# Kernel optimization log

Measured on AMD Instinct MI355X. Metric: run time of the kernel, lower is better.

Reference implementation:

```python
import jax, jax.numpy as jnp
import numpy as np

N_NODES = 50000
N_EDGES = 640000
D = 128  # input = hidden = output channels (must match for this module's forward to type-check)


def gcn_conv(x, W, b, src, dst, n):
    """PyG GCNConv: out = D^{-1/2} (A + I) D^{-1/2} (x @ W) + b.
    src = edge_index[0] (source/message sender), dst = edge_index[1] (target/aggregation index).
    """
    h = x @ W  # [n, d_out]
    loop = jnp.arange(n)
    s = jnp.concatenate([src, loop])  # add self-loops
    d = jnp.concatenate([dst, loop])
    deg = jax.ops.segment_sum(jnp.ones(s.shape[0], dtype=h.dtype), d, num_segments=n)
    dis = jax.lax.rsqrt(deg)  # deg >= 1 thanks to self-loops
    norm = dis[s] * dis[d]  # [E + n]
    msg = h[s] * norm[:, None]  # gather + scale (largest intermediate)
    return jax.ops.segment_sum(msg, d, num_segments=n) + b


def setup_inputs() -> dict:
    key = jax.random.key(0)
    ks = jax.random.split(key, 9)
    x = jax.random.normal(ks[0], (N_NODES, D), dtype=jnp.float32)
    edge_index_normal = jax.random.randint(ks[1], (2, N_EDGES), 0, N_NODES, dtype=jnp.int64 if jax.config.jax_enable_x64 else jnp.int32)
    edge_index_role = jax.random.randint(ks[2], (2, N_EDGES), 0, N_NODES, dtype=jnp.int64 if jax.config.jax_enable_x64 else jnp.int32)
    s = 1.0 / np.sqrt(D)
    W_role = jax.random.uniform(ks[3], (D, D), jnp.float32, -s, s)
    b_role = jnp.zeros((D,), jnp.float32)
    W2 = jax.random.uniform(ks[4], (D, D), jnp.float32, -s, s)
    b2 = jnp.zeros((D,), jnp.float32)
    W1 = jax.random.uniform(ks[5], (D, D), jnp.float32, -s, s)
    b1 = jnp.zeros((D,), jnp.float32)
    return {"x": x, "W_role": W_role, "b_role": b_role, "W2": W2, "b2": b2,
            "W1": W1, "b1": b1,
            "edge_index_normal": edge_index_normal, "edge_index_role": edge_index_role}


def reference(x, W_role, b_role, W2, b2, W1, b1, edge_index_normal, edge_index_role):
    n = x.shape[0]
    # conv_role on the role graph, then conv2 and conv1 on the normal graph.
    h = jax.nn.relu(gcn_conv(x, W_role, b_role, edge_index_role[0], edge_index_role[1], n))
    # dropout(p=0.5) is identity in eval mode
    h = jax.nn.relu(gcn_conv(h, W2, b2, edge_index_normal[0], edge_index_normal[1], n))
    out = gcn_conv(h, W1, b1, edge_index_normal[0], edge_index_normal[1], n)
    return out
```

## Files before the change

### kernel.cpp

```cpp
#include <hip/hip_runtime.h>
#include <hip/hip_fp16.h>

#define D 128
#define CHUNK 8192
#define BSH 7
#define BNODES 128
#define MAXNB 512
#define CAP 6144
#define PADK 136

typedef _Float16 half8 __attribute__((ext_vector_type(8)));
typedef float float4v __attribute__((ext_vector_type(4)));

__global__ __launch_bounds__(256) void p1_hist(const int* __restrict__ dst_n,
                                               const int* __restrict__ dst_r,
                                               int En, int Er,
                                               int* __restrict__ base2,
                                               int NB, int NC, int L) {
    int g = blockIdx.x / NC, c = blockIdx.x % NC;
    const int* dst = g ? dst_r : dst_n;
    int E = g ? Er : En;
    __shared__ int hist[MAXNB];
    for (int i = threadIdx.x; i < NB; i += 256) hist[i] = 0;
    __syncthreads();
    int e0 = c * CHUNK, e1 = min(e0 + CHUNK, E);
    for (int e = e0 + threadIdx.x; e < e1; e += 256)
        atomicAdd(&hist[dst[e] >> BSH], 1);
    __syncthreads();
    for (int b = threadIdx.x; b < NB; b += 256)
        base2[g * L + b * NC + c] = hist[b];
}

__global__ __launch_bounds__(1024) void scan_pass1(const int* __restrict__ data,
                                                   int* __restrict__ bsum2, int L, int nb) {
    int g = blockIdx.x / nb, b = blockIdx.x % nb;
    int i = b * 1024 + threadIdx.x;
    int v = (i < L) ? data[g * L + i] : 0;
    #pragma unroll
    for (int off = 32; off; off >>= 1) v += __shfl_down(v, off, 64);
    __shared__ int wsum[16];
    int lane = threadIdx.x & 63, wid = threadIdx.x >> 6;
    if (lane == 0) wsum[wid] = v;
    __syncthreads();
    if (threadIdx.x == 0) {
        int s = 0;
        for (int w = 0; w < 16; ++w) s += wsum[w];
        bsum2[g * 64 + b] = s;
    }
}

__global__ __launch_bounds__(128) void scan_pass2(int* __restrict__ bsum2, int nb) {
    int wid = threadIdx.x >> 6, lane = threadIdx.x & 63;
    int v = (lane < nb) ? bsum2[wid * 64 + lane] : 0;
    int incl = v;
    #pragma unroll
    for (int off = 1; off < 64; off <<= 1) {
        int t = __shfl_up(incl, off, 64);
        if (lane >= off) incl += t;
    }
    if (lane < nb) bsum2[wid * 64 + lane] = incl - v;
}

__global__ __launch_bounds__(1024) void scan_pass3(int* __restrict__ data,
                                                   const int* __restrict__ bsum2,
                                                   int L, int nb) {
    int g = blockIdx.x / nb, b = blockIdx.x % nb;
    int i = b * 1024 + threadIdx.x;
    int v = (i < L) ? data[g * L + i] : 0;
    int lane = threadIdx.x & 63, wid = threadIdx.x >> 6;
    int incl = v;
    #pragma unroll
    for (int off = 1; off < 64; off <<= 1) {
        int t = __shfl_up(incl, off, 64);
        if (lane >= off) incl += t;
    }
    __shared__ int wsum[16];
    if (lane == 63) wsum[wid] = incl;
    __syncthreads();
    if (threadIdx.x == 0) {
        int s = 0;
        for (int w = 0; w < 16; ++w) { int t = wsum[w]; wsum[w] = s; s += t; }
    }
    __syncthreads();
    if (i < L) data[g * L + i] = incl - v + wsum[wid] + bsum2[g * 64 + b];
}

__global__ __launch_bounds__(256) void p2_scatter(const int* __restrict__ src_n,
                                                  const int* __restrict__ dst_n,
                                                  const int* __restrict__ src_r,
                                                  const int* __restrict__ dst_r,
                                                  int En, int Er,
                                                  const int* __restrict__ base2,
                                                  unsigned int* __restrict__ part_n,
                                                  unsigned int* __restrict__ part_r,
                                                  int NB, int NC, int L) {
    int g = blockIdx.x / NC, c = blockIdx.x % NC;
    const int* src = g ? src_r : src_n;
    const int* dst = g ? dst_r : dst_n;
    unsigned int* part = g ? part_r : part_n;
    int E = g ? Er : En;
    __shared__ int cur[MAXNB];
    for (int b = threadIdx.x; b < NB; b += 256)
        cur[b] = base2[g * L + b * NC + c];
    __syncthreads();
    int e0 = c * CHUNK, e1 = min(e0 + CHUNK, E);
    for (int e = e0 + threadIdx.x; e < e1; e += 256) {
        int d = dst[e];
        int pos = atomicAdd(&cur[d >> BSH], 1);
        part[pos] = ((unsigned)d << 16) | (unsigned)src[e];
    }
}

__global__ __launch_bounds__(256) void p3_csr(const unsigned int* __restrict__ part_n,
                                              const unsigned int* __restrict__ part_r,
                                              const int* __restrict__ base2,
                                              int* __restrict__ rs2,
                                              float* __restrict__ dis2,
                                              unsigned short* __restrict__ csr_n,
                                              unsigned short* __restrict__ csr_r,
                                              int n, int NB, int NC, int L, int En, int Er) {
    int g = blockIdx.x / NB, b = blockIdx.x % NB;
    const unsigned int* part = g ? part_r : part_n;
    unsigned short* csr = g ? csr_r : csr_n;
    int E = g ? Er : En;
    __shared__ int deg[BNODES];
    __shared__ int cur[BNODES];
    __shared__ unsigned short buf[CAP];
    __shared__ int w0tot;
    int t = threadIdx.x;
    if (t < BNODES) deg[t] = 0;
    __syncthreads();
    int bstart = base2[g * L + b * NC];
    int bend = (b + 1 < NB) ? base2[g * L + (b + 1) * NC] : E;
    int sz = bend - bstart;
    for (int e = bstart + t; e < bend; e += 256)
        atomicAdd(&deg[(part[e] >> 16) & (BNODES - 1)], 1);
    __syncthreads();
    int incl = 0, v = 0;
    if (t < BNODES) {
        int lane = t & 63;
        v = deg[t];
        incl = v;
        #pragma unroll
        for (int off = 1; off < 64; off <<= 1) {
            int tt = __shfl_up(incl, off, 64);
            if (lane >= off) incl += tt;
        }
        if (t == 63) w0tot = incl;
    }
    __syncthreads();
    if (t < BNODES) {
        int excl = incl - v + ((t >= 64) ? w0tot : 0);
        cur[t] = excl;
        int idx = b * BNODES + t;
        if (idx < n) {
            rs2[g * (n + 1) + idx] = bstart + excl;
            dis2[g * n + idx] = rsqrtf((float)(deg[t] + 1));
        }
    }
    if (b == NB - 1 && t == 255) rs2[g * (n + 1) + n] = E;
    __syncthreads();
    if (sz <= CAP) {
        for (int e = bstart + t; e < bend; e += 256) {
            unsigned int p = part[e];
            int pos = atomicAdd(&cur[(p >> 16) & (BNODES - 1)], 1);
            buf[pos] = (unsigned short)(p & 0xffffu);
        }
        __syncthreads();
        for (int i = t; i < sz; i += 256) csr[bstart + i] = buf[i];
    } else {
        for (int e = bstart + t; e < bend; e += 256) {
            unsigned int p = part[e];
            int pos = atomicAdd(&cur[(p >> 16) & (BNODES - 1)], 1);
            csr[bstart + pos] = (unsigned short)(p & 0xffffu);
        }
    }
}

__global__ __launch_bounds__(256) void wprep(const float* __restrict__ W2,
                                             const float* __restrict__ W1,
                                             _Float16* __restrict__ Wt2,
                                             _Float16* __restrict__ Wt1) {
    int i = blockIdx.x * 256 + threadIdx.x;
    int m = i >> 14;
    int idx = i & 16383;
    int nn = idx >> 7, k = idx & 127;
    const float* W = m ? W1 : W2;
    _Float16* Wt = m ? Wt1 : Wt2;
    Wt[nn * 128 + k] = (_Float16)W[k * 128 + nn];
}


__global__ __launch_bounds__(256) void gemm_scale(const float* __restrict__ X,
                                                  const float* __restrict__ W,
                                                  const float* __restrict__ dis,
                                                  __half* __restrict__ Y, int n) {
    __shared__ float sX[128 * D];
    int t = threadIdx.x;
    int rg = t >> 4;
    int cg = (t & 15) << 3;
    int rb = blockIdx.x * 128;
    int rows = min(128, n - rb);

    float4* sX4 = (float4*)sX;
    for (int i = t; i < rows * 32; i += 256)
        sX4[i] = ((const float4*)X)[(size_t)rb * 32 + i];
    __syncthreads();

    float acc[8][8] = {};
    #pragma unroll 2
    for (int k0 = 0; k0 < D; k0 += 4) {
        float4 xr[8];
        #pragma unroll
        for (int r = 0; r < 8; ++r)
            xr[r] = *(const float4*)&sX[(rg * 8 + r) * D + k0];
        #pragma unroll
        for (int j = 0; j < 4; ++j) {
            float4 wa = *(const float4*)(W + (size_t)(k0 + j) * D + cg);
            float4 wb = *(const float4*)(W + (size_t)(k0 + j) * D + cg + 4);
            #pragma unroll
            for (int r = 0; r < 8; ++r) {
                float xv = ((const float*)&xr[r])[j];
                acc[r][0] += xv * wa.x; acc[r][1] += xv * wa.y;
                acc[r][2] += xv * wa.z; acc[r][3] += xv * wa.w;
                acc[r][4] += xv * wb.x; acc[r][5] += xv * wb.y;
                acc[r][6] += xv * wb.z; acc[r][7] += xv * wb.w;
            }
        }
    }
    #pragma unroll
    for (int r = 0; r < 8; ++r) {
        int row = rb + rg * 8 + r;
        if (row < n) {
            float dv = dis[row];
            __half2 p0 = __floats2half2_rn(acc[r][0] * dv, acc[r][1] * dv);
            __half2 p1 = __floats2half2_rn(acc[r][2] * dv, acc[r][3] * dv);
            __half2 p2 = __floats2half2_rn(acc[r][4] * dv, acc[r][5] * dv);
            __half2 p3 = __floats2half2_rn(acc[r][6] * dv, acc[r][7] * dv);
            uint4 o;
            o.x = *(unsigned*)&p0; o.y = *(unsigned*)&p1;
            o.z = *(unsigned*)&p2; o.w = *(unsigned*)&p3;
            *(uint4*)(Y + (size_t)row * D + cg) = o;
        }
    }
}

__global__ __launch_bounds__(256) void gemm_mfma(const _Float16* __restrict__ Xh,
                                                 const _Float16* __restrict__ Wt,
                                                 const float* __restrict__ dis,
                                                 _Float16* __restrict__ Y, int n) {
    __shared__ _Float16 sA[128 * PADK];
    __shared__ _Float16 sB[128 * PADK];
    int t = threadIdx.x;
    int rb = blockIdx.x * 128;
    int rows = min(128, n - rb);

    for (int i = t; i < 128 * 16; i += 256) {
        int r = i >> 4, s = i & 15;
        *(uint4*)&sB[r * PADK + s * 8] = ((const uint4*)Wt)[i];
    }
    for (int i = t; i < rows * 16; i += 256) {
        int r = i >> 4, s = i & 15;
        *(uint4*)&sA[r * PADK + s * 8] = ((const uint4*)(Xh + (size_t)rb * D))[i];
    }
    if (rows < 128) {
        for (int i = rows * 16 + t; i < 128 * 16; i += 256) {
            int r = i >> 4, s = i & 15;
            *(uint4*)&sA[r * PADK + s * 8] = make_uint4(0, 0, 0, 0);
        }
    }
    __syncthreads();

    int w = t >> 6, lane = t & 63;
    int quad = lane >> 4, l16 = lane & 15;
    float4v acc[2][8];
    #pragma unroll
    for (int rt = 0; rt < 2; ++rt)
        #pragma unroll
        for (int ct = 0; ct < 8; ++ct)
            acc[rt][ct] = (float4v){0.f, 0.f, 0.f, 0.f};

    #pragma unroll
    for (int k0 = 0; k0 < 128; k0 += 32) {
        half8 a0 = *(half8*)&sA[(w * 32 + l16) * PADK + k0 + quad * 8];
        half8 a1 = *(half8*)&sA[(w * 32 + 16 + l16) * PADK + k0 + quad * 8];
        #pragma unroll
        for (int ct = 0; ct < 8; ++ct) {
            half8 b = *(half8*)&sB[(ct * 16 + l16) * PADK + k0 + quad * 8];
            acc[0][ct] = __builtin_amdgcn_mfma_f32_16x16x32_f16(a0, b, acc[0][ct], 0, 0, 0);
            acc[1][ct] = __builtin_amdgcn_mfma_f32_16x16x32_f16(a1, b, acc[1][ct], 0, 0, 0);
        }
    }
    #pragma unroll
    for (int rt = 0; rt < 2; ++rt) {
        #pragma unroll
        for (int r = 0; r < 4; ++r) {
            int row = rb + w * 32 + rt * 16 + quad * 4 + r;
            if (row < n) {
                float dv = dis[row];
                #pragma unroll
                for (int ct = 0; ct < 8; ++ct)
                    Y[(size_t)row * D + ct * 16 + l16] = (_Float16)(acc[rt][ct][r] * dv);
            }
        }
    }
}

__global__ __launch_bounds__(256) void aggregate(const __half* __restrict__ g,
                                                 const int* __restrict__ rs,
                                                 const unsigned short* __restrict__ csr,
                                                 const float* __restrict__ dis,
                                                 const float* __restrict__ bias,
                                                 float* __restrict__ outf,
                                                 _Float16* __restrict__ outh,
                                                 int n, int do_relu, int write_half) {
    int v = blockIdx.x * 16 + (threadIdx.x >> 4);
    if (v >= n) return;
    int l16 = threadIdx.x & 15;
    const uint4* g4 = (const uint4*)g;
    float acc[8];
    {
        uint4 raw = g4[(size_t)v * 16 + l16];
        float2 f0 = __half22float2(*(__half2*)&raw.x);
        float2 f1 = __half22float2(*(__half2*)&raw.y);
        float2 f2 = __half22float2(*(__half2*)&raw.z);
        float2 f3 = __half22float2(*(__half2*)&raw.w);
        acc[0] = f0.x; acc[1] = f0.y; acc[2] = f1.x; acc[3] = f1.y;
        acc[4] = f2.x; acc[5] = f2.y; acc[6] = f3.x; acc[7] = f3.y;
    }
    int e = rs[v], end = rs[v + 1];
    while (e < end) {
        int m = min(16, end - e);
        int sid = (e + l16 < end) ? (int)csr[e + l16] : 0;
        int j = 0;
        for (; j + 7 < m; j += 8) {
            uint4 raw[8];
            #pragma unroll
            for (int u = 0; u < 8; ++u) {
                int s = __shfl(sid, j + u, 16);
                raw[u] = g4[(size_t)s * 16 + l16];
            }
            #pragma unroll
            for (int u = 0; u < 8; ++u) {
                float2 f0 = __half22float2(*(__half2*)&raw[u].x);
                float2 f1 = __half22float2(*(__half2*)&raw[u].y);
                float2 f2 = __half22float2(*(__half2*)&raw[u].z);
                float2 f3 = __half22float2(*(__half2*)&raw[u].w);
                acc[0] += f0.x; acc[1] += f0.y; acc[2] += f1.x; acc[3] += f1.y;
                acc[4] += f2.x; acc[5] += f2.y; acc[6] += f3.x; acc[7] += f3.y;
            }
        }
        for (; j + 3 < m; j += 4) {
            uint4 raw[4];
            #pragma unroll
            for (int u = 0; u < 4; ++u) {
                int s = __shfl(sid, j + u, 16);
                raw[u] = g4[(size_t)s * 16 + l16];
            }
            #pragma unroll
            for (int u = 0; u < 4; ++u) {
                float2 f0 = __half22float2(*(__half2*)&raw[u].x);
                float2 f1 = __half22float2(*(__half2*)&raw[u].y);
                float2 f2 = __half22float2(*(__half2*)&raw[u].z);
                float2 f3 = __half22float2(*(__half2*)&raw[u].w);
                acc[0] += f0.x; acc[1] += f0.y; acc[2] += f1.x; acc[3] += f1.y;
                acc[4] += f2.x; acc[5] += f2.y; acc[6] += f3.x; acc[7] += f3.y;
            }
        }
        for (; j < m; ++j) {
            int s = __shfl(sid, j, 16);
            uint4 raw = g4[(size_t)s * 16 + l16];
            float2 f0 = __half22float2(*(__half2*)&raw.x);
            float2 f1 = __half22float2(*(__half2*)&raw.y);
            float2 f2 = __half22float2(*(__half2*)&raw.z);
            float2 f3 = __half22float2(*(__half2*)&raw.w);
            acc[0] += f0.x; acc[1] += f0.y; acc[2] += f1.x; acc[3] += f1.y;
            acc[4] += f2.x; acc[5] += f2.y; acc[6] += f3.x; acc[7] += f3.y;
        }
        e += m;
    }
    float dv = dis[v];
    const float4* b4 = (const float4*)bias;
    float4 ba = b4[2 * l16], bb = b4[2 * l16 + 1];
    float o[8];
    o[0] = dv * acc[0] + ba.x; o[1] = dv * acc[1] + ba.y;
    o[2] = dv * acc[2] + ba.z; o[3] = dv * acc[3] + ba.w;
    o[4] = dv * acc[4] + bb.x; o[5] = dv * acc[5] + bb.y;
    o[6] = dv * acc[6] + bb.z; o[7] = dv * acc[7] + bb.w;
    if (do_relu) {
        #pragma unroll
        for (int i = 0; i < 8; ++i) o[i] = fmaxf(o[i], 0.f);
    }
    if (write_half) {
        __half2 p0 = __floats2half2_rn(o[0], o[1]);
        __half2 p1 = __floats2half2_rn(o[2], o[3]);
        __half2 p2 = __floats2half2_rn(o[4], o[5]);
        __half2 p3 = __floats2half2_rn(o[6], o[7]);
        uint4 pk;
        pk.x = *(unsigned*)&p0; pk.y = *(unsigned*)&p1;
        pk.z = *(unsigned*)&p2; pk.w = *(unsigned*)&p3;
        ((uint4*)outh)[(size_t)v * 16 + l16] = pk;
    } else {
        float4* orow = (float4*)(outf + (size_t)v * D);
        orow[2 * l16] = make_float4(o[0], o[1], o[2], o[3]);
        orow[2 * l16 + 1] = make_float4(o[4], o[5], o[6], o[7]);
    }
}


extern "C" void kernel_launch(void* const* d_in, const int* in_sizes, int n_in,
                              void* d_out, int out_size, void* d_ws, size_t ws_size,
                              hipStream_t stream) {
    const float* x      = (const float*)d_in[0];
    const float* W_role = (const float*)d_in[1];
    const float* b_role = (const float*)d_in[2];
    const float* W2     = (const float*)d_in[3];
    const float* b2     = (const float*)d_in[4];
    const float* W1     = (const float*)d_in[5];
    const float* b1     = (const float*)d_in[6];
    const int*   ein    = (const int*)d_in[7];
    const int*   eir    = (const int*)d_in[8];

    int n  = in_sizes[0] / D;
    int En = in_sizes[7] / 2;
    int Er = in_sizes[8] / 2;
    const int* src_n = ein;
    const int* dst_n = ein + En;
    const int* src_r = eir;
    const int* dst_r = eir + Er;
    float* out = (float*)d_out;

    int NB = (n + BNODES - 1) >> BSH;
    int Emax = En > Er ? En : Er;
    int NC = (Emax + CHUNK - 1) / CHUNK;
    int L  = NB * NC;
    int nb_scan = (L + 1023) / 1024;

    char* p = (char*)d_ws;
    auto alloc = [&](size_t bytes) { char* r = p; p += (bytes + 255) & ~(size_t)255; return r; };
    __half*         gbuf   = (__half*)alloc((size_t)n * D * sizeof(__half));
    _Float16*       hbuf   = (_Float16*)alloc((size_t)n * D * sizeof(_Float16));
    _Float16*       Wt2    = (_Float16*)alloc((size_t)D * D * sizeof(_Float16));
    _Float16*       Wt1    = (_Float16*)alloc((size_t)D * D * sizeof(_Float16));
    float*          dis2   = (float*)alloc((size_t)2 * n * sizeof(float));
    int*            rs2    = (int*)alloc((size_t)2 * (n + 1) * sizeof(int));
    int*            base2  = (int*)alloc((size_t)2 * L * sizeof(int));
    int*            bsum2  = (int*)alloc(512);
    unsigned int*   part_n = (unsigned int*)alloc((size_t)En * sizeof(unsigned int));
    unsigned int*   part_r = (unsigned int*)alloc((size_t)Er * sizeof(unsigned int));
    unsigned short* csr    = (unsigned short*)alloc((size_t)(En + Er) * sizeof(unsigned short));
    float* dis_n = dis2;
    float* dis_r = dis2 + n;
    int*   rs_n  = rs2;
    int*   rs_r  = rs2 + (n + 1);
    unsigned short* csr_n = csr;
    unsigned short* csr_r = csr + En;

    p1_hist<<<2 * NC, 256, 0, stream>>>(dst_n, dst_r, En, Er, base2, NB, NC, L);
    scan_pass1<<<2 * nb_scan, 1024, 0, stream>>>(base2, bsum2, L, nb_scan);
    scan_pass2<<<1, 128, 0, stream>>>(bsum2, nb_scan);
    scan_pass3<<<2 * nb_scan, 1024, 0, stream>>>(base2, bsum2, L, nb_scan);
    p2_scatter<<<2 * NC, 256, 0, stream>>>(src_n, dst_n, src_r, dst_r, En, Er,
                                           base2, part_n, part_r, NB, NC, L);
    p3_csr<<<2 * NB, 256, 0, stream>>>(part_n, part_r, base2, rs2, dis2,
                                       csr_n, csr_r, n, NB, NC, L, En, Er);
    wprep<<<128, 256, 0, stream>>>(W2, W1, Wt2, Wt1);

    int gblk = (n + 127) / 128;
    int ablk = (n + 15) / 16;
    gemm_scale<<<gblk, 256, 0, stream>>>(x, W_role, dis_r, gbuf, n);
    aggregate<<<ablk, 256, 0, stream>>>(gbuf, rs_r, csr_r, dis_r, b_role,
                                        nullptr, hbuf, n, 1, 1);
    gemm_mfma<<<gblk, 256, 0, stream>>>(hbuf, Wt2, dis_n, (_Float16*)gbuf, n);
    aggregate<<<ablk, 256, 0, stream>>>(gbuf, rs_n, csr_n, dis_n, b2,
                                        nullptr, hbuf, n, 1, 1);
    gemm_mfma<<<gblk, 256, 0, stream>>>(hbuf, Wt1, dis_n, (_Float16*)gbuf, n);
    aggregate<<<ablk, 256, 0, stream>>>(gbuf, rs_n, csr_n, dis_n, b1,
                                        out, nullptr, n, 0, 0);
}
```

Measured before the change: 270.0 us.

## Fuse CSR preprocessing and weight prep into one cooperative kernel

Merges the histogram, three-pass scan, scatter, CSR build and weight transpose/convert kernels into one cooperatively launched kernel separated by grid-wide syncs. The scan is rewritten to 256 threads with 4 elements each. The aim is to remove the launch and inter-kernel drain overhead of seven small kernels. In exchange, the CSR build stage now runs in a grid-stride loop over only 2*NC blocks instead of one block per bucket, which lowers parallelism, and each grid.sync adds its own cost.

```diff
diff --git a/kernel.cpp b/kernel.cpp
--- a/kernel.cpp
+++ b/kernel.cpp
@@ -1,5 +1,8 @@
 #include <hip/hip_runtime.h>
 #include <hip/hip_fp16.h>
+#include <hip/hip_cooperative_groups.h>
+
+namespace cg = cooperative_groups;
 
 #define D 128
 #define CHUNK 8192
@@ -12,182 +15,199 @@
 typedef _Float16 half8 __attribute__((ext_vector_type(8)));
 typedef float float4v __attribute__((ext_vector_type(4)));
 
-__global__ __launch_bounds__(256) void p1_hist(const int* __restrict__ dst_n,
-                                               const int* __restrict__ dst_r,
-                                               int En, int Er,
-                                               int* __restrict__ base2,
-                                               int NB, int NC, int L) {
-    int g = blockIdx.x / NC, c = blockIdx.x % NC;
-    const int* dst = g ? dst_r : dst_n;
-    int E = g ? Er : En;
-    __shared__ int hist[MAXNB];
-    for (int i = threadIdx.x; i < NB; i += 256) hist[i] = 0;
-    __syncthreads();
-    int e0 = c * CHUNK, e1 = min(e0 + CHUNK, E);
-    for (int e = e0 + threadIdx.x; e < e1; e += 256)
-        atomicAdd(&hist[dst[e] >> BSH], 1);
-    __syncthreads();
-    for (int b = threadIdx.x; b < NB; b += 256)
-        base2[g * L + b * NC + c] = hist[b];
-}
-
-__global__ __launch_bounds__(1024) void scan_pass1(const int* __restrict__ data,
-                                                   int* __restrict__ bsum2, int L, int nb) {
-    int g = blockIdx.x / nb, b = blockIdx.x % nb;
-    int i = b * 1024 + threadIdx.x;
-    int v = (i < L) ? data[g * L + i] : 0;
-    #pragma unroll
-    for (int off = 32; off; off >>= 1) v += __shfl_down(v, off, 64);
-    __shared__ int wsum[16];
-    int lane = threadIdx.x & 63, wid = threadIdx.x >> 6;
-    if (lane == 0) wsum[wid] = v;
-    __syncthreads();
-    if (threadIdx.x == 0) {
+__global__ __launch_bounds__(256) void preproc(
+    const int* __restrict__ src_n, const int* __restrict__ dst_n,
+    const int* __restrict__ src_r, const int* __restrict__ dst_r,
+    int En, int Er,
+    const float* __restrict__ W2, const float* __restrict__ W1,
+    _Float16* __restrict__ Wt2, _Float16* __restrict__ Wt1,
+    int* __restrict__ base2, int* __restrict__ bsum2,
+    unsigned int* __restrict__ part_n, unsigned int* __restrict__ part_r,
+    int* __restrict__ rs2, float* __restrict__ dis2,
+    unsigned short* __restrict__ csr_n, unsigned short* __restrict__ csr_r,
+    int n, int NB, int NC, int L, int nb_scan)
+{
+    cg::grid_group grid = cg::this_grid();
+    __shared__ __align__(16) char smem[14336];
+    int t = threadIdx.x;
+    int nblk = gridDim.x;
+
+    for (int i = blockIdx.x * 256 + t; i < 2 * 128 * 128; i += nblk * 256) {
+        int m = i >> 14, idx = i & 16383;
+        int nn = idx >> 7, k = idx & 127;
+        const float* W = m ? W1 : W2;
+        _Float16* Wt = m ? Wt1 : Wt2;
+        Wt[nn * 128 + k] = (_Float16)W[k * 128 + nn];
+    }
+
+    {
+        int g = blockIdx.x / NC, c = blockIdx.x % NC;
+        int* hist = (int*)smem;
+        const int* dst = g ? dst_r : dst_n;
+        int E = g ? Er : En;
+        for (int i = t; i < NB; i += 256) hist[i] = 0;
+        __syncthreads();
+        int e0 = c * CHUNK, e1 = min(e0 + CHUNK, E);
+        for (int e = e0 + t; e < e1; e += 256)
+            atomicAdd(&hist[dst[e] >> BSH], 1);
+        __syncthreads();
+        for (int b = t; b < NB; b += 256)
+            base2[g * L + b * NC + c] = hist[b];
+    }
+    grid.sync();
+
+    for (int task = blockIdx.x; task < 2 * nb_scan; task += nblk) {
+        int g = task / nb_scan, b = task % nb_scan;
+        int base = b * 1024 + t * 4;
         int s = 0;
-        for (int w = 0; w < 16; ++w) s += wsum[w];
-        bsum2[g * 64 + b] = s;
-    }
-}
-
-__global__ __launch_bounds__(128) void scan_pass2(int* __restrict__ bsum2, int nb) {
-    int wid = threadIdx.x >> 6, lane = threadIdx.x & 63;
-    int v = (lane < nb) ? bsum2[wid * 64 + lane] : 0;
-    int incl = v;
-    #pragma unroll
-    for (int off = 1; off < 64; off <<= 1) {
-        int t = __shfl_up(incl, off, 64);
-        if (lane >= off) incl += t;
-    }
-    if (lane < nb) bsum2[wid * 64 + lane] = incl - v;
-}
-
-__global__ __launch_bounds__(1024) void scan_pass3(int* __restrict__ data,
-                                                   const int* __restrict__ bsum2,
-                                                   int L, int nb) {
-    int g = blockIdx.x / nb, b = blockIdx.x % nb;
-    int i = b * 1024 + threadIdx.x;
-    int v = (i < L) ? data[g * L + i] : 0;
-    int lane = threadIdx.x & 63, wid = threadIdx.x >> 6;
-    int incl = v;
-    #pragma unroll
-    for (int off = 1; off < 64; off <<= 1) {
-        int t = __shfl_up(incl, off, 64);
-        if (lane >= off) incl += t;
-    }
-    __shared__ int wsum[16];
-    if (lane == 63) wsum[wid] = incl;
-    __syncthreads();
-    if (threadIdx.x == 0) {
-        int s = 0;
-        for (int w = 0; w < 16; ++w) { int t = wsum[w]; wsum[w] = s; s += t; }
-    }
-    __syncthreads();
-    if (i < L) data[g * L + i] = incl - v + wsum[wid] + bsum2[g * 64 + b];
-}
-
-__global__ __launch_bounds__(256) void p2_scatter(const int* __restrict__ src_n,
-                                                  const int* __restrict__ dst_n,
-                                                  const int* __restrict__ src_r,
-                                                  const int* __restrict__ dst_r,
-                                                  int En, int Er,
-                                                  const int* __restrict__ base2,
-                                                  unsigned int* __restrict__ part_n,
-                                                  unsigned int* __restrict__ part_r,
-                                                  int NB, int NC, int L) {
-    int g = blockIdx.x / NC, c = blockIdx.x % NC;
-    const int* src = g ? src_r : src_n;
-    const int* dst = g ? dst_r : dst_n;
-    unsigned int* part = g ? part_r : part_n;
-    int E = g ? Er : En;
-    __shared__ int cur[MAXNB];
-    for (int b = threadIdx.x; b < NB; b += 256)
-        cur[b] = base2[g * L + b * NC + c];
-    __syncthreads();
-    int e0 = c * CHUNK, e1 = min(e0 + CHUNK, E);
-    for (int e = e0 + threadIdx.x; e < e1; e += 256) {
-        int d = dst[e];
-        int pos = atomicAdd(&cur[d >> BSH], 1);
-        part[pos] = ((unsigned)d << 16) | (unsigned)src[e];
-    }
-}
-
-__global__ __launch_bounds__(256) void p3_csr(const unsigned int* __restrict__ part_n,
-                                              const unsigned int* __restrict__ part_r,
-                                              const int* __restrict__ base2,
-                                              int* __restrict__ rs2,
-                                              float* __restrict__ dis2,
-                                              unsigned short* __restrict__ csr_n,
-                                              unsigned short* __restrict__ csr_r,
-                                              int n, int NB, int NC, int L, int En, int Er) {
-    int g = blockIdx.x / NB, b = blockIdx.x % NB;
-    const unsigned int* part = g ? part_r : part_n;
-    unsigned short* csr = g ? csr_r : csr_n;
-    int E = g ? Er : En;
-    __shared__ int deg[BNODES];
-    __shared__ int cur[BNODES];
-    __shared__ unsigned short buf[CAP];
-    __shared__ int w0tot;
-    int t = threadIdx.x;
-    if (t < BNODES) deg[t] = 0;
-    __syncthreads();
-    int bstart = base2[g * L + b * NC];
-    int bend = (b + 1 < NB) ? base2[g * L + (b + 1) * NC] : E;
-    int sz = bend - bstart;
-    for (int e = bstart + t; e < bend; e += 256)
-        atomicAdd(&deg[(part[e] >> 16) & (BNODES - 1)], 1);
-    __syncthreads();
-    int incl = 0, v = 0;
-    if (t < BNODES) {
-        int lane = t & 63;
-        v = deg[t];
-        incl = v;
+        #pragma unroll
+        for (int j = 0; j < 4; ++j) {
+            int i = base + j;
+            if (i < L) s += base2[g * L + i];
+        }
+        int lane = t & 63, wid = t >> 6;
+        #pragma unroll
+        for (int off = 32; off; off >>= 1) s += __shfl_down(s, off, 64);
+        int* wsum = (int*)smem;
+        if (lane == 0) wsum[wid] = s;
+        __syncthreads();
+        if (t == 0) {
+            int tot = 0;
+            for (int w = 0; w < 4; ++w) tot += wsum[w];
+            bsum2[g * 64 + b] = tot;
+        }
+        __syncthreads();
+    }
+    grid.sync();
+
+    if (blockIdx.x == 0 && t < 128) {
+        int wid = t >> 6, lane = t & 63;
+        int v = (lane < nb_scan) ? bsum2[wid * 64 + lane] : 0;
+        int incl = v;
         #pragma unroll
         for (int off = 1; off < 64; off <<= 1) {
             int tt = __shfl_up(incl, off, 64);
             if (lane >= off) incl += tt;
         }
-        if (t == 63) w0tot = incl;
-    }
-    __syncthreads();
-    if (t < BNODES) {
-        int excl = incl - v + ((t >= 64) ? w0tot : 0);
-        cur[t] = excl;
-        int idx = b * BNODES + t;
-        if (idx < n) {
-            rs2[g * (n + 1) + idx] = bstart + excl;
-            dis2[g * n + idx] = rsqrtf((float)(deg[t] + 1));
-        }
-    }
-    if (b == NB - 1 && t == 255) rs2[g * (n + 1) + n] = E;
-    __syncthreads();
-    if (sz <= CAP) {
-        for (int e = bstart + t; e < bend; e += 256) {
-            unsigned int p = part[e];
-            int pos = atomicAdd(&cur[(p >> 16) & (BNODES - 1)], 1);
-            buf[pos] = (unsigned short)(p & 0xffffu);
-        }
-        __syncthreads();
-        for (int i = t; i < sz; i += 256) csr[bstart + i] = buf[i];
-    } else {
-        for (int e = bstart + t; e < bend; e += 256) {
-            unsigned int p = part[e];
-            int pos = atomicAdd(&cur[(p >> 16) & (BNODES - 1)], 1);
-            csr[bstart + pos] = (unsigned short)(p & 0xffffu);
-        }
-    }
-}
-
-__global__ __launch_bounds__(256) void wprep(const float* __restrict__ W2,
-                                             const float* __restrict__ W1,
-                                             _Float16* __restrict__ Wt2,
-                                             _Float16* __restrict__ Wt1) {
-    int i = blockIdx.x * 256 + threadIdx.x;
-    int m = i >> 14;
-    int idx = i & 16383;
-    int nn = idx >> 7, k = idx & 127;
-    const float* W = m ? W1 : W2;
-    _Float16* Wt = m ? Wt1 : Wt2;
-    Wt[nn * 128 + k] = (_Float16)W[k * 128 + nn];
+        if (lane < nb_scan) bsum2[wid * 64 + lane] = incl - v;
+    }
+    grid.sync();
+
+    for (int task = blockIdx.x; task < 2 * nb_scan; task += nblk) {
+        int g = task / nb_scan, b = task % nb_scan;
+        int base = b * 1024 + t * 4;
+        int v[4];
+        #pragma unroll
+        for (int j = 0; j < 4; ++j) {
+            int i = base + j;
+            v[j] = (i < L) ? base2[g * L + i] : 0;
+        }
+        int tsum = v[0] + v[1] + v[2] + v[3];
+        int lane = t & 63, wid = t >> 6;
+        int incl = tsum;
+        #pragma unroll
+        for (int off = 1; off < 64; off <<= 1) {
+            int tt = __shfl_up(incl, off, 64);
+            if (lane >= off) incl += tt;
+        }
+        int* wsum = (int*)smem;
+        if (lane == 63) wsum[wid] = incl;
+        __syncthreads();
+        if (t == 0) {
+            int s = 0;
+            for (int w = 0; w < 4; ++w) { int tt = wsum[w]; wsum[w] = s; s += tt; }
+        }
+        __syncthreads();
+        int excl = incl - tsum + wsum[wid] + bsum2[g * 64 + b];
+        #pragma unroll
+        for (int j = 0; j < 4; ++j) {
+            int i = base + j;
+            if (i < L) base2[g * L + i] = excl;
+            excl += v[j];
+        }
+        __syncthreads();
+    }
+    grid.sync();
+
+    {
+        int g = blockIdx.x / NC, c = blockIdx.x % NC;
+        const int* src = g ? src_r : src_n;
+        const int* dst = g ? dst_r : dst_n;
+        unsigned int* part = g ? part_r : part_n;
+        int E = g ? Er : En;
+        int* cur = (int*)smem;
+        for (int b = t; b < NB; b += 256)
+            cur[b] = base2[g * L + b * NC + c];
+        __syncthreads();
+        int e0 = c * CHUNK, e1 = min(e0 + CHUNK, E);
+        for (int e = e0 + t; e < e1; e += 256) {
+            int d = dst[e];
+            int pos = atomicAdd(&cur[d >> BSH], 1);
+            part[pos] = ((unsigned)d << 16) | (unsigned)src[e];
+        }
+    }
+    grid.sync();
+
+    {
+        int* deg = (int*)smem;
+        int* cur = deg + 128;
+        int* w0tot = cur + 128;
+        unsigned short* buf = (unsigned short*)(w0tot + 4);
+        for (int task = blockIdx.x; task < 2 * NB; task += nblk) {
+            int g = task / NB, b = task % NB;
+            const unsigned int* part = g ? part_r : part_n;
+            unsigned short* csr = g ? csr_r : csr_n;
+            int E = g ? Er : En;
+            if (t < BNODES) deg[t] = 0;
+            __syncthreads();
+            int bstart = base2[g * L + b * NC];
+            int bend = (b + 1 < NB) ? base2[g * L + (b + 1) * NC] : E;
+            int sz = bend - bstart;
+            for (int e = bstart + t; e < bend; e += 256)
+                atomicAdd(&deg[(part[e] >> 16) & (BNODES - 1)], 1);
+            __syncthreads();
+            int incl = 0, v = 0;
+            if (t < BNODES) {
+                int lane = t & 63;
+                v = deg[t];
+                incl = v;
+                #pragma unroll
+                for (int off = 1; off < 64; off <<= 1) {
+                    int tt = __shfl_up(incl, off, 64);
+                    if (lane >= off) incl += tt;
+                }
+                if (t == 63) w0tot[0] = incl;
+            }
+            __syncthreads();
+            if (t < BNODES) {
+                int excl = incl - v + ((t >= 64) ? w0tot[0] : 0);
+                cur[t] = excl;
+                int idx = b * BNODES + t;
+                if (idx < n) {
+                    rs2[g * (n + 1) + idx] = bstart + excl;
+                    dis2[g * n + idx] = rsqrtf((float)(deg[t] + 1));
+                }
+            }
+            if (b == NB - 1 && t == 255) rs2[g * (n + 1) + n] = E;
+            __syncthreads();
+            if (sz <= CAP) {
+                for (int e = bstart + t; e < bend; e += 256) {
+                    unsigned int p = part[e];
+                    int pos = atomicAdd(&cur[(p >> 16) & (BNODES - 1)], 1);
+                    buf[pos] = (unsigned short)(p & 0xffffu);
+                }
+                __syncthreads();
+                for (int i = t; i < sz; i += 256) csr[bstart + i] = buf[i];
+            } else {
+                for (int e = bstart + t; e < bend; e += 256) {
+                    unsigned int p = part[e];
+                    int pos = atomicAdd(&cur[(p >> 16) & (BNODES - 1)], 1);
+                    csr[bstart + pos] = (unsigned short)(p & 0xffffu);
+                }
+            }
+            __syncthreads();
+        }
+    }
 }
 
 
@@ -456,15 +476,20 @@
     unsigned short* csr_n = csr;
     unsigned short* csr_r = csr + En;
 
-    p1_hist<<<2 * NC, 256, 0, stream>>>(dst_n, dst_r, En, Er, base2, NB, NC, L);
-    scan_pass1<<<2 * nb_scan, 1024, 0, stream>>>(base2, bsum2, L, nb_scan);
-    scan_pass2<<<1, 128, 0, stream>>>(bsum2, nb_scan);
-    scan_pass3<<<2 * nb_scan, 1024, 0, stream>>>(base2, bsum2, L, nb_scan);
-    p2_scatter<<<2 * NC, 256, 0, stream>>>(src_n, dst_n, src_r, dst_r, En, Er,
-                                           base2, part_n, part_r, NB, NC, L);
-    p3_csr<<<2 * NB, 256, 0, stream>>>(part_n, part_r, base2, rs2, dis2,
-                                       csr_n, csr_r, n, NB, NC, L, En, Er);
-    wprep<<<128, 256, 0, stream>>>(W2, W1, Wt2, Wt1);
+    {
+        void* args[] = {
+            (void*)&src_n, (void*)&dst_n, (void*)&src_r, (void*)&dst_r,
+            (void*)&En, (void*)&Er,
+            (void*)&W2, (void*)&W1, (void*)&Wt2, (void*)&Wt1,
+            (void*)&base2, (void*)&bsum2,
+            (void*)&part_n, (void*)&part_r,
+            (void*)&rs2, (void*)&dis2,
+            (void*)&csr_n, (void*)&csr_r,
+            (void*)&n, (void*)&NB, (void*)&NC, (void*)&L, (void*)&nb_scan
+        };
+        hipLaunchCooperativeKernel((const void*)preproc, dim3(2 * NC), dim3(256),
+                                   args, 0, stream);
+    }
 
     int gblk = (n + 127) / 128;
     int ablk = (n + 15) / 16;
```

After: 399.5 us. 48.0% more time.

## Use MFMA for first-layer GEMM and fuse small prep kernels

Applied to the files above, without the earlier changes.

Replaces the scalar FP32 first-layer GEMM with an MFMA fp16 kernel that converts x to half while staging it in shared memory. The weight transpose/convert for all three matrices moves into the histogram kernel, and the second scan pass is folded into the third, which removes two launches. CHUNK is halved so there are more histogram/scatter blocks. Converting x to fp16 before the first GEMM adds rounding error, and the CHUNK change alters how parallel the partitioning passes are.

```diff
diff --git a/kernel.cpp b/kernel.cpp
--- a/kernel.cpp
+++ b/kernel.cpp
@@ -2,7 +2,7 @@
 #include <hip/hip_fp16.h>
 
 #define D 128
-#define CHUNK 8192
+#define CHUNK 4096
 #define BSH 7
 #define BNODES 128
 #define MAXNB 512
@@ -15,8 +15,21 @@
 __global__ __launch_bounds__(256) void p1_hist(const int* __restrict__ dst_n,
                                                const int* __restrict__ dst_r,
                                                int En, int Er,
+                                               const float* __restrict__ Wr,
+                                               const float* __restrict__ W2,
+                                               const float* __restrict__ W1,
+                                               _Float16* __restrict__ Wtr,
+                                               _Float16* __restrict__ Wt2,
+                                               _Float16* __restrict__ Wt1,
                                                int* __restrict__ base2,
                                                int NB, int NC, int L) {
+    for (int i = blockIdx.x * 256 + threadIdx.x; i < 3 * 128 * 128; i += gridDim.x * 256) {
+        int m = i >> 14, idx = i & 16383;
+        int nn = idx >> 7, k = idx & 127;
+        const float* W = (m == 0) ? Wr : (m == 1) ? W2 : W1;
+        _Float16* Wt = (m == 0) ? Wtr : (m == 1) ? Wt2 : Wt1;
+        Wt[nn * 128 + k] = (_Float16)W[k * 128 + nn];
+    }
     int g = blockIdx.x / NC, c = blockIdx.x % NC;
     const int* dst = g ? dst_r : dst_n;
     int E = g ? Er : En;
@@ -49,22 +62,22 @@
     }
 }
 
-__global__ __launch_bounds__(128) void scan_pass2(int* __restrict__ bsum2, int nb) {
-    int wid = threadIdx.x >> 6, lane = threadIdx.x & 63;
-    int v = (lane < nb) ? bsum2[wid * 64 + lane] : 0;
-    int incl = v;
-    #pragma unroll
-    for (int off = 1; off < 64; off <<= 1) {
-        int t = __shfl_up(incl, off, 64);
-        if (lane >= off) incl += t;
-    }
-    if (lane < nb) bsum2[wid * 64 + lane] = incl - v;
-}
-
 __global__ __launch_bounds__(1024) void scan_pass3(int* __restrict__ data,
                                                    const int* __restrict__ bsum2,
                                                    int L, int nb) {
     int g = blockIdx.x / nb, b = blockIdx.x % nb;
+    __shared__ int sOffset;
+    if (threadIdx.x < 64) {
+        int lane = threadIdx.x;
+        int v = (lane < nb) ? bsum2[g * 64 + lane] : 0;
+        int incl = v;
+        #pragma unroll
+        for (int off = 1; off < 64; off <<= 1) {
+            int t = __shfl_up(incl, off, 64);
+            if (lane >= off) incl += t;
+        }
+        if (lane == b) sOffset = incl - v;
+    }
     int i = b * 1024 + threadIdx.x;
     int v = (i < L) ? data[g * L + i] : 0;
     int lane = threadIdx.x & 63, wid = threadIdx.x >> 6;
@@ -82,7 +95,7 @@
         for (int w = 0; w < 16; ++w) { int t = wsum[w]; wsum[w] = s; s += t; }
     }
     __syncthreads();
-    if (i < L) data[g * L + i] = incl - v + wsum[wid] + bsum2[g * 64 + b];
+    if (i < L) data[g * L + i] = incl - v + wsum[wid] + sOffset;
 }
 
 __global__ __launch_bounds__(256) void p2_scatter(const int* __restrict__ src_n,
@@ -177,73 +190,6 @@
     }
 }
 
-__global__ __launch_bounds__(256) void wprep(const float* __restrict__ W2,
-                                             const float* __restrict__ W1,
-                                             _Float16* __restrict__ Wt2,
-                                             _Float16* __restrict__ Wt1) {
-    int i = blockIdx.x * 256 + threadIdx.x;
-    int m = i >> 14;
-    int idx = i & 16383;
-    int nn = idx >> 7, k = idx & 127;
-    const float* W = m ? W1 : W2;
-    _Float16* Wt = m ? Wt1 : Wt2;
-    Wt[nn * 128 + k] = (_Float16)W[k * 128 + nn];
-}
-
-
-__global__ __launch_bounds__(256) void gemm_scale(const float* __restrict__ X,
-                                                  const float* __restrict__ W,
-                                                  const float* __restrict__ dis,
-                                                  __half* __restrict__ Y, int n) {
-    __shared__ float sX[128 * D];
-    int t = threadIdx.x;
-    int rg = t >> 4;
-    int cg = (t & 15) << 3;
-    int rb = blockIdx.x * 128;
-    int rows = min(128, n - rb);
-
-    float4* sX4 = (float4*)sX;
-    for (int i = t; i < rows * 32; i += 256)
-        sX4[i] = ((const float4*)X)[(size_t)rb * 32 + i];
-    __syncthreads();
-
-    float acc[8][8] = {};
-    #pragma unroll 2
-    for (int k0 = 0; k0 < D; k0 += 4) {
-        float4 xr[8];
-        #pragma unroll
-        for (int r = 0; r < 8; ++r)
-            xr[r] = *(const float4*)&sX[(rg * 8 + r) * D + k0];
-        #pragma unroll
-        for (int j = 0; j < 4; ++j) {
-            float4 wa = *(const float4*)(W + (size_t)(k0 + j) * D + cg);
-            float4 wb = *(const float4*)(W + (size_t)(k0 + j) * D + cg + 4);
-            #pragma unroll
-            for (int r = 0; r < 8; ++r) {
-                float xv = ((const float*)&xr[r])[j];
-                acc[r][0] += xv * wa.x; acc[r][1] += xv * wa.y;
-                acc[r][2] += xv * wa.z; acc[r][3] += xv * wa.w;
-                acc[r][4] += xv * wb.x; acc[r][5] += xv * wb.y;
-                acc[r][6] += xv * wb.z; acc[r][7] += xv * wb.w;
-            }
-        }
-    }
-    #pragma unroll
-    for (int r = 0; r < 8; ++r) {
-        int row = rb + rg * 8 + r;
-        if (row < n) {
-            float dv = dis[row];
-            __half2 p0 = __floats2half2_rn(acc[r][0] * dv, acc[r][1] * dv);
-            __half2 p1 = __floats2half2_rn(acc[r][2] * dv, acc[r][3] * dv);
-            __half2 p2 = __floats2half2_rn(acc[r][4] * dv, acc[r][5] * dv);
-            __half2 p3 = __floats2half2_rn(acc[r][6] * dv, acc[r][7] * dv);
-            uint4 o;
-            o.x = *(unsigned*)&p0; o.y = *(unsigned*)&p1;
-            o.z = *(unsigned*)&p2; o.w = *(unsigned*)&p3;
-            *(uint4*)(Y + (size_t)row * D + cg) = o;
-        }
-    }
-}
 
 __global__ __launch_bounds__(256) void gemm_mfma(const _Float16* __restrict__ Xh,
                                                  const _Float16* __restrict__ Wt,
@@ -262,6 +208,72 @@
     for (int i = t; i < rows * 16; i += 256) {
         int r = i >> 4, s = i & 15;
         *(uint4*)&sA[r * PADK + s * 8] = ((const uint4*)(Xh + (size_t)rb * D))[i];
+    }
+    if (rows < 128) {
+        for (int i = rows * 16 + t; i < 128 * 16; i += 256) {
+            int r = i >> 4, s = i & 15;
+            *(uint4*)&sA[r * PADK + s * 8] = make_uint4(0, 0, 0, 0);
+        }
+    }
+    __syncthreads();
+
+    int w = t >> 6, lane = t & 63;
+    int quad = lane >> 4, l16 = lane & 15;
+    float4v acc[2][8];
+    #pragma unroll
+    for (int rt = 0; rt < 2; ++rt)
+        #pragma unroll
+        for (int ct = 0; ct < 8; ++ct)
+            acc[rt][ct] = (float4v){0.f, 0.f, 0.f, 0.f};
+
+    #pragma unroll
+    for (int k0 = 0; k0 < 128; k0 += 32) {
+        half8 a0 = *(half8*)&sA[(w * 32 + l16) * PADK + k0 + quad * 8];
+        half8 a1 = *(half8*)&sA[(w * 32 + 16 + l16) * PADK + k0 + quad * 8];
+        #pragma unroll
+        for (int ct = 0; ct < 8; ++ct) {
+            half8 b = *(half8*)&sB[(ct * 16 + l16) * PADK + k0 + quad * 8];
+            acc[0][ct] = __builtin_amdgcn_mfma_f32_16x16x32_f16(a0, b, acc[0][ct], 0, 0, 0);
+            acc[1][ct] = __builtin_amdgcn_mfma_f32_16x16x32_f16(a1, b, acc[1][ct], 0, 0, 0);
+        }
+    }
+    #pragma unroll
+    for (int rt = 0; rt < 2; ++rt) {
+        #pragma unroll
+        for (int r = 0; r < 4; ++r) {
+            int row = rb + w * 32 + rt * 16 + quad * 4 + r;
+            if (row < n) {
+                float dv = dis[row];
+                #pragma unroll
+                for (int ct = 0; ct < 8; ++ct)
+                    Y[(size_t)row * D + ct * 16 + l16] = (_Float16)(acc[rt][ct][r] * dv);
+            }
+        }
+    }
+}
+
+__global__ __launch_bounds__(256) void gemm_mfma_x(const float* __restrict__ X,
+                                                   const _Float16* __restrict__ Wt,
+                                                   const float* __restrict__ dis,
+                                                   _Float16* __restrict__ Y, int n) {
+    __shared__ _Float16 sA[128 * PADK];
+    __shared__ _Float16 sB[128 * PADK];
+    int t = threadIdx.x;
+    int rb = blockIdx.x * 128;
+    int rows = min(128, n - rb);
+
+    for (int i = t; i < 128 * 16; i += 256) {
+        int r = i >> 4, s = i & 15;
+        *(uint4*)&sB[r * PADK + s * 8] = ((const uint4*)Wt)[i];
+    }
+    for (int i = t; i < rows * 16; i += 256) {
+        int r = i >> 4, s = i & 15;
+        const float* xp = X + (size_t)(rb + r) * D + s * 8;
+        float4 a = *(const float4*)xp;
+        float4 b = *(const float4*)(xp + 4);
+        _Float16 h[8] = {(_Float16)a.x, (_Float16)a.y, (_Float16)a.z, (_Float16)a.w,
+                         (_Float16)b.x, (_Float16)b.y, (_Float16)b.z, (_Float16)b.w};
+        *(half8*)&sA[r * PADK + s * 8] = *(half8*)h;
     }
     if (rows < 128) {
         for (int i = rows * 16 + t; i < 128 * 16; i += 256) {
@@ -440,6 +452,7 @@
     auto alloc = [&](size_t bytes) { char* r = p; p += (bytes + 255) & ~(size_t)255; return r; };
     __half*         gbuf   = (__half*)alloc((size_t)n * D * sizeof(__half));
     _Float16*       hbuf   = (_Float16*)alloc((size_t)n * D * sizeof(_Float16));
+    _Float16*       Wtr    = (_Float16*)alloc((size_t)D * D * sizeof(_Float16));
     _Float16*       Wt2    = (_Float16*)alloc((size_t)D * D * sizeof(_Float16));
     _Float16*       Wt1    = (_Float16*)alloc((size_t)D * D * sizeof(_Float16));
     float*          dis2   = (float*)alloc((size_t)2 * n * sizeof(float));
@@ -456,19 +469,19 @@
     unsigned short* csr_n = csr;
     unsigned short* csr_r = csr + En;
 
-    p1_hist<<<2 * NC, 256, 0, stream>>>(dst_n, dst_r, En, Er, base2, NB, NC, L);
+    p1_hist<<<2 * NC, 256, 0, stream>>>(dst_n, dst_r, En, Er,
+                                        W_role, W2, W1, Wtr, Wt2, Wt1,
+                                        base2, NB, NC, L);
     scan_pass1<<<2 * nb_scan, 1024, 0, stream>>>(base2, bsum2, L, nb_scan);
-    scan_pass2<<<1, 128, 0, stream>>>(bsum2, nb_scan);
     scan_pass3<<<2 * nb_scan, 1024, 0, stream>>>(base2, bsum2, L, nb_scan);
     p2_scatter<<<2 * NC, 256, 0, stream>>>(src_n, dst_n, src_r, dst_r, En, Er,
                                            base2, part_n, part_r, NB, NC, L);
     p3_csr<<<2 * NB, 256, 0, stream>>>(part_n, part_r, base2, rs2, dis2,
                                        csr_n, csr_r, n, NB, NC, L, En, Er);
-    wprep<<<128, 256, 0, stream>>>(W2, W1, Wt2, Wt1);
 
     int gblk = (n + 127) / 128;
     int ablk = (n + 15) / 16;
-    gemm_scale<<<gblk, 256, 0, stream>>>(x, W_role, dis_r, gbuf, n);
+    gemm_mfma_x<<<gblk, 256, 0, stream>>>(x, Wtr, dis_r, (_Float16*)gbuf, n);
     aggregate<<<ablk, 256, 0, stream>>>(gbuf, rs_r, csr_r, dis_r, b_role,
                                         nullptr, hbuf, n, 1, 1);
     gemm_mfma<<<gblk, 256, 0, stream>>>(hbuf, Wt2, dis_n, (_Float16*)gbuf, n);
```

After: 240.3 us. 11.0% less time.
